# Kernel tuning notes

Measured on AMD Instinct MI355X. Metric: run time of the kernel, lower is better.

## Reference

```python
import jax, jax.numpy as jnp
import numpy as np

B, LQ, LA, H = 32, 1024, 1024, 512
NEG = -1e7


def setup_inputs() -> dict:
    key = jax.random.key(0)
    kq, ka, ku = jax.random.split(key, 3)
    q = jax.random.normal(kq, (B, LQ, H), dtype=jnp.float32)
    a = jax.random.normal(ka, (B, LA, H), dtype=jnp.float32)
    U = 0.02 * jax.random.normal(ku, (H, H), dtype=jnp.float32)  # init.normal(std=0.02)
    q_mask = jnp.ones((B, LQ, 1), dtype=jnp.float32)
    a_mask = jnp.ones((B, LA, 1), dtype=jnp.float32)
    return {"q": q, "a": a, "U": U, "q_mask": q_mask, "a_mask": a_mask}


def reference(q, a, U, q_mask, a_mask):
    # mask[b,i,j] = q_mask[b,i] * a_mask[b,j]  (nonzero => valid)
    mask = jnp.matmul(q_mask, jnp.swapaxes(a_mask, 1, 2)) > 0  # [B,LQ,LA] bool
    # bilinear score X = q @ U @ a^T
    qU = jnp.einsum('bqh,hk->bqk', q, U)
    X = jnp.einsum('bqk,bak->bqa', qU, a)  # [B,LQ,LA]
    X = jnp.where(mask, X, NEG)
    I = jax.nn.sigmoid(X)
    att_a2q = jnp.max(jax.nn.softmax(I, axis=-1), axis=-1)  # [B,LQ]
    att_q2a = jnp.max(jax.nn.softmax(I, axis=-2), axis=-2)  # [B,LA]
    q_attn = jnp.einsum('blh,bl->bh', q, att_a2q)  # [B,H]
    a_attn = jnp.einsum('blh,bl->bh', a, att_q2a)  # [B,H]
    return q_attn, a_attn
```

## Files before the change

### kernel.cpp

```cpp
#include <hip/hip_runtime.h>

typedef __attribute__((ext_vector_type(8))) short bf16x8;
typedef __attribute__((ext_vector_type(4))) float f32x4;
typedef unsigned short u16;
typedef unsigned int u32;

#define NLOG2E -1.44269504088896f
#define LOG2E   1.44269504088896f

__device__ __forceinline__ float bf2f(u16 x) {
  union { u32 u; float f; } v; v.u = ((u32)x) << 16; return v.f;
}
__device__ __forceinline__ u16 f2b(float f) {
  union { float f; u32 u; } v; v.f = f;
  return (u16)((v.u + 0x7FFFu + ((v.u >> 16) & 1u)) >> 16);
}
__device__ __forceinline__ bool inputs_are_bf16(const void* qmask) {
  return *(const u32*)qmask == 0x3F803F80u;
}
__device__ __forceinline__ u32 fkey(float f) {
  u32 b = __float_as_uint(f);
  return (b >> 31) ? ~b : (b | 0x80000000u);
}
__device__ __forceinline__ float fkey_inv(u32 k) {
  u32 b = (k & 0x80000000u) ? (k ^ 0x80000000u) : ~k;
  return __uint_as_float(b);
}

__global__ __launch_bounds__(256) void prep_all(
    const void* __restrict__ q, const void* __restrict__ a,
    const void* __restrict__ U, const void* __restrict__ qmask,
    u16* __restrict__ qb, u16* __restrict__ ab, u16* __restrict__ Ut,
    u32* __restrict__ stats)
{
  const bool bf = inputs_are_bf16(qmask);
  const int t = threadIdx.x;
  __shared__ u16 tile[64][65];
  if (blockIdx.x < 8192) {
    const int idx = blockIdx.x * 256 + t;
    if (idx < 131072) stats[idx] = (idx < 65536) ? 0u : 0xFFFFFFFFu;
    const size_t base = (size_t)idx * 8;
    if (bf) {
      *(bf16x8*)&qb[base] = ((const bf16x8*)q)[idx];
      *(bf16x8*)&ab[base] = ((const bf16x8*)a)[idx];
    } else {
      const float4* qf = (const float4*)q;
      const float4* af = (const float4*)a;
      float4 x0 = qf[2 * idx], x1 = qf[2 * idx + 1];
      u16 o[8] = {f2b(x0.x), f2b(x0.y), f2b(x0.z), f2b(x0.w),
                  f2b(x1.x), f2b(x1.y), f2b(x1.z), f2b(x1.w)};
      *(bf16x8*)&qb[base] = *(bf16x8*)o;
      float4 y0 = af[2 * idx], y1 = af[2 * idx + 1];
      u16 p[8] = {f2b(y0.x), f2b(y0.y), f2b(y0.z), f2b(y0.w),
                  f2b(y1.x), f2b(y1.y), f2b(y1.z), f2b(y1.w)};
      *(bf16x8*)&ab[base] = *(bf16x8*)p;
    }
  } else {
    const int bb = blockIdx.x - 8192;
    const int bx = bb & 7, by = bb >> 3;
    #pragma unroll
    for (int i = 0; i < 16; i++) {
      int r = i * 4 + (t >> 6);
      int c = t & 63;
      size_t gi = (size_t)(by * 64 + r) * 512 + bx * 64 + c;
      tile[c][r] = bf ? ((const u16*)U)[gi] : f2b(((const float*)U)[gi]);
    }
    __syncthreads();
    #pragma unroll
    for (int i = 0; i < 16; i++) {
      int r = i * 4 + (t >> 6);
      int c = t & 63;
      Ut[(size_t)(bx * 64 + r) * 512 + by * 64 + c] = tile[r][c];
    }
  }
}

template<int EPI>
__global__ __launch_bounds__(256) void gemm_bt(
    const u16* __restrict__ A, const u16* __restrict__ B,
    u16* __restrict__ C, float scaleC,
    size_t strideA, size_t strideB,
    const void* __restrict__ q_mask, const void* __restrict__ a_mask,
    float* __restrict__ rowsumA, float* __restrict__ colsumA,
    u32* __restrict__ rowkeyA, u32* __restrict__ colkeyA)
{
  __shared__ __align__(16) char smem[33792];
  u16* As = (u16*)smem;
  u16* Bs = (u16*)(smem + 16384);
  float* redS = (float*)smem;
  float* redM = (float*)(smem + 16896);
  __shared__ float qp[128], ap[128];

  const int tid  = threadIdx.x;
  const int lane = tid & 63;
  const int wave = tid >> 6;
  const int wr = wave >> 1, wc = wave & 1;
  const int l15 = lane & 15, lq = lane >> 4;
  const int rsub = lane >> 3;
  const int csw  = (lane & 7) ^ rsub;

  const u16* Ab = A + strideA * blockIdx.z + (size_t)blockIdx.y * 128 * 512;
  const u16* Bb = B + strideB * blockIdx.z + (size_t)blockIdx.x * 128 * 512;

  if (EPI) {
    const bool bf = inputs_are_bf16(q_mask);
    if (tid < 128) {
      int gi = blockIdx.z * 1024 + blockIdx.y * 128 + tid;
      float v = bf ? bf2f(((const u16*)q_mask)[gi]) : ((const float*)q_mask)[gi];
      qp[tid] = (v > 0.f) ? 0.f : 1e30f;
    } else if (tid < 256) {
      int gj = blockIdx.z * 1024 + blockIdx.x * 128 + (tid - 128);
      float v = bf ? bf2f(((const u16*)a_mask)[gj]) : ((const float*)a_mask)[gj];
      ap[tid - 128] = (v > 0.f) ? 0.f : 1e30f;
    }
  }

  f32x4 acc[4][4];
  #pragma unroll
  for (int i = 0; i < 4; i++)
    #pragma unroll
    for (int j = 0; j < 4; j++) {
      f32x4 z = {0.f, 0.f, 0.f, 0.f};
      acc[i][j] = z;
    }

  for (int k0 = 0; k0 < 512; k0 += 64) {
    #pragma unroll
    for (int i = 0; i < 4; i++) {
      const int r0 = wave * 32 + i * 8;
      const size_t go = (size_t)(r0 + rsub) * 512 + k0 + csw * 8;
      __builtin_amdgcn_global_load_lds(
          (const __attribute__((address_space(1))) void*)(Ab + go),
          (__attribute__((address_space(3))) void*)&As[r0 * 64], 16, 0, 0);
      __builtin_amdgcn_global_load_lds(
          (const __attribute__((address_space(1))) void*)(Bb + go),
          (__attribute__((address_space(3))) void*)&Bs[r0 * 64], 16, 0, 0);
    }
    __syncthreads();
    #pragma unroll
    for (int ks = 0; ks < 64; ks += 32) {
      const int cx = ((ks >> 3) + lq) ^ (l15 & 7);
      bf16x8 af[4], bfr[4];
      #pragma unroll
      for (int tt = 0; tt < 4; tt++) {
        af[tt]  = *(const bf16x8*)&As[(wr * 64 + tt * 16 + l15) * 64 + cx * 8];
        bfr[tt] = *(const bf16x8*)&Bs[(wc * 64 + tt * 16 + l15) * 64 + cx * 8];
      }
      #pragma unroll
      for (int mt = 0; mt < 4; mt++)
        #pragma unroll
        for (int nt = 0; nt < 4; nt++)
          acc[mt][nt] = __builtin_amdgcn_mfma_f32_16x16x32_bf16(af[mt], bfr[nt], acc[mt][nt], 0, 0, 0);
    }
    __syncthreads();
  }

  if (!EPI) {
    u16* Cb = C + (size_t)blockIdx.y * 128 * 512 + blockIdx.x * 128;
    #pragma unroll
    for (int mt = 0; mt < 4; mt++)
      #pragma unroll
      for (int nt = 0; nt < 4; nt++)
        #pragma unroll
        for (int r = 0; r < 4; r++) {
          int row = wr * 64 + mt * 16 + lq * 4 + r;
          int col = wc * 64 + nt * 16 + l15;
          Cb[(size_t)row * 512 + col] = f2b(scaleC * acc[mt][nt][r]);
        }
  } else {
    const int gi0 = blockIdx.z * 1024 + blockIdx.y * 128;
    const int gj0 = blockIdx.z * 1024 + blockIdx.x * 128;
    float apen[4];
    #pragma unroll
    for (int nt = 0; nt < 4; nt++) apen[nt] = ap[wc * 64 + nt * 16 + l15];

    float csum[4] = {0.f, 0.f, 0.f, 0.f};
    float cmin[4] = {3e38f, 3e38f, 3e38f, 3e38f};
    #pragma unroll
    for (int mt = 0; mt < 4; mt++) {
      #pragma unroll
      for (int r = 0; r < 4; r++) {
        const int row = wr * 64 + mt * 16 + lq * 4 + r;
        const float rowpen = qp[row];
        float rsm = 0.f, rmn = 3e38f;
        #pragma unroll
        for (int nt = 0; nt < 4; nt++) {
          float y = acc[mt][nt][r] + (rowpen + apen[nt]);
          float u = __builtin_amdgcn_exp2f(y);
          float s = __builtin_amdgcn_rcpf(1.f + u);
          float e = __builtin_amdgcn_exp2f(LOG2E * s);
          rsm += e;
          csum[nt] += e;
          rmn = fminf(rmn, y);
          cmin[nt] = fminf(cmin[nt], y);
        }
        redS[row * 33 + l15 + 16 * wc] = rsm;
        redM[row * 33 + l15 + 16 * wc] = rmn;
      }
    }
    #pragma unroll
    for (int nt = 0; nt < 4; nt++) {
      float cs = csum[nt], cm = cmin[nt];
      cs += __shfl_xor(cs, 16); cm = fminf(cm, __shfl_xor(cm, 16));
      cs += __shfl_xor(cs, 32); cm = fminf(cm, __shfl_xor(cm, 32));
      if (lane < 16) {
        int gj = gj0 + wc * 64 + nt * 16 + l15;
        atomicAdd(&colsumA[gj], cs);
        atomicMin(&colkeyA[gj], fkey(cm));
      }
    }
    __syncthreads();
    if (tid < 128) {
      float s = 0.f;
      #pragma unroll
      for (int j = 0; j < 32; j++) s += redS[tid * 33 + j];
      atomicAdd(&rowsumA[gi0 + tid], s);
    } else {
      const int row = tid - 128;
      float m = 3e38f;
      #pragma unroll
      for (int j = 0; j < 32; j++) m = fminf(m, redM[row * 33 + j]);
      atomicMin(&rowkeyA[gi0 + row], fkey(m));
    }
  }
}

__global__ __launch_bounds__(256) void partial_kernel(
    const u16* __restrict__ qb, const u16* __restrict__ ab,
    const u32* __restrict__ stats, float* __restrict__ outp)
{
  __shared__ float att[128];
  const int tid = threadIdx.x;
  const int hc = blockIdx.x, seg = blockIdx.y;
  const int b = blockIdx.z >> 1, half = blockIdx.z & 1;
  const float* sm = (const float*)stats + half * 32768 + b * 1024 + seg * 128;
  const u32* ky = stats + 65536 + half * 32768 + b * 1024 + seg * 128;
  if (tid < 128) {
    float ymin = fkey_inv(ky[tid]);
    float Imax = __builtin_amdgcn_rcpf(1.f + __builtin_amdgcn_exp2f(ymin));
    att[tid] = __expf(Imax) * __builtin_amdgcn_rcpf(sm[tid]);
  }
  __syncthreads();
  const u16* src = (half ? ab : qb) + (size_t)b * 524288 + (size_t)seg * 128 * 512;
  const int h = hc * 256 + tid;
  float acc = 0.f;
  #pragma unroll 8
  for (int i = 0; i < 128; i++) acc += bf2f(src[(size_t)i * 512 + h]) * att[i];
  outp[(size_t)seg * 32768 + half * 16384 + b * 512 + h] = acc;
}

__global__ __launch_bounds__(256) void final_sum(const float* __restrict__ outp,
                                                 float* __restrict__ out) {
  const int idx = blockIdx.x * 256 + threadIdx.x;
  float s = 0.f;
  #pragma unroll
  for (int k = 0; k < 8; k++) s += outp[(size_t)k * 32768 + idx];
  out[idx] = s;
}

extern "C" void kernel_launch(void* const* d_in, const int* in_sizes, int n_in,
                              void* d_out, int out_size, void* d_ws, size_t ws_size,
                              hipStream_t stream) {
  const void* q  = d_in[0];
  const void* a  = d_in[1];
  const void* U  = d_in[2];
  const void* qm = d_in[3];
  const void* am = d_in[4];
  float* out = (float*)d_out;

  char* ws = (char*)d_ws;
  u16* qb    = (u16*)ws;
  u16* ab    = (u16*)(ws + 33554432);
  u16* qU    = (u16*)(ws + 67108864);
  u16* Ut    = (u16*)(ws + 100663296);
  u32* stats = (u32*)(ws + 101187584);
  float* outp  = (float*)(ws + 101711872);
  float* rowsumA = (float*)stats;
  float* colsumA = (float*)stats + 32768;
  u32* rowkeyA = stats + 65536;
  u32* colkeyA = stats + 98304;

  prep_all<<<dim3(8256), dim3(256), 0, stream>>>(q, a, U, qm, qb, ab, Ut, stats);
  gemm_bt<0><<<dim3(4, 256, 1), dim3(256), 0, stream>>>(
      qb, Ut, qU, NLOG2E, (size_t)0, (size_t)0, qm, am,
      rowsumA, colsumA, rowkeyA, colkeyA);
  gemm_bt<1><<<dim3(8, 8, 32), dim3(256), 0, stream>>>(
      qU, ab, (u16*)nullptr, 1.f, (size_t)524288, (size_t)524288, qm, am,
      rowsumA, colsumA, rowkeyA, colkeyA);
  partial_kernel<<<dim3(2, 8, 64), dim3(256), 0, stream>>>(qb, ab, stats, outp);
  final_sum<<<dim3(128), dim3(256), 0, stream>>>(outp, out);
}
```

Baseline: 266.1 us.

## Load A fragments directly to registers, stage C via LDS, drop final_sum kernel

The GEMM now reads the A operand straight from global memory into registers instead of staging it in LDS, and only B goes through LDS. The non-epilogue GEMM writes its output tile through a padded LDS buffer so global stores become 16-byte vectors. The mask penalties are folded into the accumulator initial values. The final_sum kernel is removed: partial_kernel atomically adds into an output that prep_all zeroes. This saves one launch and an LDS round-trip, at the cost of uncoalesced global A loads, an extra barrier, and nondeterministic float atomics.

```diff
diff --git a/kernel.cpp b/kernel.cpp
--- a/kernel.cpp
+++ b/kernel.cpp
@@ -31,7 +31,7 @@
     const void* __restrict__ q, const void* __restrict__ a,
     const void* __restrict__ U, const void* __restrict__ qmask,
     u16* __restrict__ qb, u16* __restrict__ ab, u16* __restrict__ Ut,
-    u32* __restrict__ stats)
+    u32* __restrict__ stats, float* __restrict__ out)
 {
   const bool bf = inputs_are_bf16(qmask);
   const int t = threadIdx.x;
@@ -39,6 +39,7 @@
   if (blockIdx.x < 8192) {
     const int idx = blockIdx.x * 256 + t;
     if (idx < 131072) stats[idx] = (idx < 65536) ? 0u : 0xFFFFFFFFu;
+    if (idx < 32768) out[idx] = 0.f;
     const size_t base = (size_t)idx * 8;
     if (bf) {
       *(bf16x8*)&qb[base] = ((const bf16x8*)q)[idx];
@@ -84,12 +85,13 @@
     float* __restrict__ rowsumA, float* __restrict__ colsumA,
     u32* __restrict__ rowkeyA, u32* __restrict__ colkeyA)
 {
-  __shared__ __align__(16) char smem[33792];
-  u16* As = (u16*)smem;
-  u16* Bs = (u16*)(smem + 16384);
+  __shared__ __align__(16) char smem[35840];
+  u16* Bs = (u16*)smem;
+  u16* Ct = (u16*)smem;
   float* redS = (float*)smem;
   float* redM = (float*)(smem + 16896);
-  __shared__ float qp[128], ap[128];
+  float* qp = (float*)(smem + 34816);
+  float* ap = (float*)(smem + 35328);
 
   const int tid  = threadIdx.x;
   const int lane = tid & 63;
@@ -108,21 +110,34 @@
       int gi = blockIdx.z * 1024 + blockIdx.y * 128 + tid;
       float v = bf ? bf2f(((const u16*)q_mask)[gi]) : ((const float*)q_mask)[gi];
       qp[tid] = (v > 0.f) ? 0.f : 1e30f;
-    } else if (tid < 256) {
+    } else {
       int gj = blockIdx.z * 1024 + blockIdx.x * 128 + (tid - 128);
       float v = bf ? bf2f(((const u16*)a_mask)[gj]) : ((const float*)a_mask)[gj];
       ap[tid - 128] = (v > 0.f) ? 0.f : 1e30f;
     }
+    __syncthreads();
   }
 
   f32x4 acc[4][4];
-  #pragma unroll
-  for (int i = 0; i < 4; i++)
-    #pragma unroll
-    for (int j = 0; j < 4; j++) {
-      f32x4 z = {0.f, 0.f, 0.f, 0.f};
-      acc[i][j] = z;
-    }
+  if (EPI) {
+    #pragma unroll
+    for (int mt = 0; mt < 4; mt++)
+      #pragma unroll
+      for (int nt = 0; nt < 4; nt++) {
+        float cp = ap[wc * 64 + nt * 16 + l15];
+        #pragma unroll
+        for (int r = 0; r < 4; r++)
+          acc[mt][nt][r] = qp[wr * 64 + mt * 16 + lq * 4 + r] + cp;
+      }
+  } else {
+    #pragma unroll
+    for (int i = 0; i < 4; i++)
+      #pragma unroll
+      for (int j = 0; j < 4; j++) {
+        f32x4 z = {0.f, 0.f, 0.f, 0.f};
+        acc[i][j] = z;
+      }
+  }
 
   for (int k0 = 0; k0 < 512; k0 += 64) {
     #pragma unroll
@@ -130,33 +145,35 @@
       const int r0 = wave * 32 + i * 8;
       const size_t go = (size_t)(r0 + rsub) * 512 + k0 + csw * 8;
       __builtin_amdgcn_global_load_lds(
-          (const __attribute__((address_space(1))) void*)(Ab + go),
-          (__attribute__((address_space(3))) void*)&As[r0 * 64], 16, 0, 0);
-      __builtin_amdgcn_global_load_lds(
           (const __attribute__((address_space(1))) void*)(Bb + go),
           (__attribute__((address_space(3))) void*)&Bs[r0 * 64], 16, 0, 0);
     }
+    bf16x8 afr[2][4];
+    #pragma unroll
+    for (int h = 0; h < 2; h++)
+      #pragma unroll
+      for (int tt = 0; tt < 4; tt++)
+        afr[h][tt] = *(const bf16x8*)&Ab[(size_t)(wr * 64 + tt * 16 + l15) * 512
+                                         + k0 + h * 32 + lq * 8];
     __syncthreads();
     #pragma unroll
     for (int ks = 0; ks < 64; ks += 32) {
       const int cx = ((ks >> 3) + lq) ^ (l15 & 7);
-      bf16x8 af[4], bfr[4];
-      #pragma unroll
-      for (int tt = 0; tt < 4; tt++) {
-        af[tt]  = *(const bf16x8*)&As[(wr * 64 + tt * 16 + l15) * 64 + cx * 8];
+      bf16x8 bfr[4];
+      #pragma unroll
+      for (int tt = 0; tt < 4; tt++)
         bfr[tt] = *(const bf16x8*)&Bs[(wc * 64 + tt * 16 + l15) * 64 + cx * 8];
-      }
       #pragma unroll
       for (int mt = 0; mt < 4; mt++)
         #pragma unroll
         for (int nt = 0; nt < 4; nt++)
-          acc[mt][nt] = __builtin_amdgcn_mfma_f32_16x16x32_bf16(af[mt], bfr[nt], acc[mt][nt], 0, 0, 0);
+          acc[mt][nt] = __builtin_amdgcn_mfma_f32_16x16x32_bf16(afr[ks >> 5][mt], bfr[nt],
+                                                                acc[mt][nt], 0, 0, 0);
     }
     __syncthreads();
   }
 
   if (!EPI) {
-    u16* Cb = C + (size_t)blockIdx.y * 128 * 512 + blockIdx.x * 128;
     #pragma unroll
     for (int mt = 0; mt < 4; mt++)
       #pragma unroll
@@ -165,15 +182,19 @@
         for (int r = 0; r < 4; r++) {
           int row = wr * 64 + mt * 16 + lq * 4 + r;
           int col = wc * 64 + nt * 16 + l15;
-          Cb[(size_t)row * 512 + col] = f2b(scaleC * acc[mt][nt][r]);
+          Ct[row * 136 + col] = f2b(scaleC * acc[mt][nt][r]);
         }
+    __syncthreads();
+    u16* Cb = C + (size_t)blockIdx.y * 128 * 512 + blockIdx.x * 128;
+    #pragma unroll
+    for (int i = 0; i < 8; i++) {
+      int c = tid + i * 256;
+      int row = c >> 4, cc = c & 15;
+      *(bf16x8*)&Cb[(size_t)row * 512 + cc * 8] = *(const bf16x8*)&Ct[row * 136 + cc * 8];
+    }
   } else {
     const int gi0 = blockIdx.z * 1024 + blockIdx.y * 128;
     const int gj0 = blockIdx.z * 1024 + blockIdx.x * 128;
-    float apen[4];
-    #pragma unroll
-    for (int nt = 0; nt < 4; nt++) apen[nt] = ap[wc * 64 + nt * 16 + l15];
-
     float csum[4] = {0.f, 0.f, 0.f, 0.f};
     float cmin[4] = {3e38f, 3e38f, 3e38f, 3e38f};
     #pragma unroll
@@ -181,11 +202,10 @@
       #pragma unroll
       for (int r = 0; r < 4; r++) {
         const int row = wr * 64 + mt * 16 + lq * 4 + r;
-        const float rowpen = qp[row];
         float rsm = 0.f, rmn = 3e38f;
         #pragma unroll
         for (int nt = 0; nt < 4; nt++) {
-          float y = acc[mt][nt][r] + (rowpen + apen[nt]);
+          float y = acc[mt][nt][r];
           float u = __builtin_amdgcn_exp2f(y);
           float s = __builtin_amdgcn_rcpf(1.f + u);
           float e = __builtin_amdgcn_exp2f(LOG2E * s);
@@ -227,7 +247,7 @@
 
 __global__ __launch_bounds__(256) void partial_kernel(
     const u16* __restrict__ qb, const u16* __restrict__ ab,
-    const u32* __restrict__ stats, float* __restrict__ outp)
+    const u32* __restrict__ stats, float* __restrict__ out)
 {
   __shared__ float att[128];
   const int tid = threadIdx.x;
@@ -246,16 +266,7 @@
   float acc = 0.f;
   #pragma unroll 8
   for (int i = 0; i < 128; i++) acc += bf2f(src[(size_t)i * 512 + h]) * att[i];
-  outp[(size_t)seg * 32768 + half * 16384 + b * 512 + h] = acc;
-}
-
-__global__ __launch_bounds__(256) void final_sum(const float* __restrict__ outp,
-                                                 float* __restrict__ out) {
-  const int idx = blockIdx.x * 256 + threadIdx.x;
-  float s = 0.f;
-  #pragma unroll
-  for (int k = 0; k < 8; k++) s += outp[(size_t)k * 32768 + idx];
-  out[idx] = s;
+  atomicAdd(&out[half * 16384 + b * 512 + h], acc);
 }
 
 extern "C" void kernel_launch(void* const* d_in, const int* in_sizes, int n_in,
@@ -274,19 +285,17 @@
   u16* qU    = (u16*)(ws + 67108864);
   u16* Ut    = (u16*)(ws + 100663296);
   u32* stats = (u32*)(ws + 101187584);
-  float* outp  = (float*)(ws + 101711872);
   float* rowsumA = (float*)stats;
   float* colsumA = (float*)stats + 32768;
   u32* rowkeyA = stats + 65536;
   u32* colkeyA = stats + 98304;
 
-  prep_all<<<dim3(8256), dim3(256), 0, stream>>>(q, a, U, qm, qb, ab, Ut, stats);
+  prep_all<<<dim3(8256), dim3(256), 0, stream>>>(q, a, U, qm, qb, ab, Ut, stats, out);
   gemm_bt<0><<<dim3(4, 256, 1), dim3(256), 0, stream>>>(
       qb, Ut, qU, NLOG2E, (size_t)0, (size_t)0, qm, am,
       rowsumA, colsumA, rowkeyA, colkeyA);
   gemm_bt<1><<<dim3(8, 8, 32), dim3(256), 0, stream>>>(
       qU, ab, (u16*)nullptr, 1.f, (size_t)524288, (size_t)524288, qm, am,
       rowsumA, colsumA, rowkeyA, colkeyA);
-  partial_kernel<<<dim3(2, 8, 64), dim3(256), 0, stream>>>(qb, ab, stats, outp);
-  final_sum<<<dim3(128), dim3(256), 0, stream>>>(outp, out);
-}
+  partial_kernel<<<dim3(2, 8, 64), dim3(256), 0, stream>>>(qb, ab, stats, out);
+}
```

New measurement: 302.1 us. 13.5% more time.
